# Optimization experiments

Measured on AMD Instinct MI355X. Metric: run time of the kernel, lower is better.

Reference implementation:

```python
import jax, jax.numpy as jnp
import numpy as np

IN_DIM = 256
HID = 512
PAT = 10
B = 512
BN_EPS = 1e-5


def setup_inputs() -> dict:
    key = jax.random.key(0)
    ks = jax.random.split(key, 16)
    s = 0.05
    return {
        "x": jax.random.normal(ks[0], (B, IN_DIM), jnp.float32),
        # pattern_detector params
        "W1": jax.random.normal(ks[1], (HID, IN_DIM), jnp.float32) * s,
        "b1": jax.random.normal(ks[2], (HID,), jnp.float32) * s,
        "bn_gamma": 1.0 + jax.random.normal(ks[3], (HID,), jnp.float32) * s,
        "bn_beta": jax.random.normal(ks[4], (HID,), jnp.float32) * s,
        "bn_mean": jax.random.normal(ks[5], (HID,), jnp.float32) * s,
        "bn_var": jnp.ones((HID,), jnp.float32),
        "W2": jax.random.normal(ks[6], (HID // 2, HID), jnp.float32) * s,
        "b2": jax.random.normal(ks[7], (HID // 2,), jnp.float32) * s,
        "W3": jax.random.normal(ks[8], (PAT, HID // 2), jnp.float32) * s,
        "b3": jax.random.normal(ks[9], (PAT,), jnp.float32) * s,
        # similarity_layer params; first Linear weight [HID, 2*IN_DIM] split into
        # the half acting on x_i (Ws1_a) and the half acting on x_j (Ws1_b)
        "Ws1_a": jax.random.normal(ks[10], (HID, IN_DIM), jnp.float32) * s,
        "Ws1_b": jax.random.normal(ks[11], (HID, IN_DIM), jnp.float32) * s,
        "bs1": jax.random.normal(ks[12], (HID,), jnp.float32) * s,
        "ws2": jax.random.normal(ks[13], (HID,), jnp.float32) * s,
        "bs2": jax.random.normal(ks[14], (), jnp.float32) * s,
    }


def reference(x, W1, b1, bn_gamma, bn_beta, bn_mean, bn_var, W2, b2, W3, b3,
              Ws1_a, Ws1_b, bs1, ws2, bs2):
    # --- pattern_detector MLP (eval mode: BN uses running stats, dropout off) ---
    h = x @ W1.T + b1                                    # [B, HID]
    h = bn_gamma * (h - bn_mean) * jax.lax.rsqrt(bn_var + BN_EPS) + bn_beta
    h = jax.nn.relu(h)
    h2 = jax.nn.relu(h @ W2.T + b2)                      # [B, HID//2]
    pattern_scores = h2 @ W3.T + b3                      # [B, PAT]
    pattern_probs = jax.nn.softmax(pattern_scores, axis=-1)

    # --- pairwise similarity: sim(i,j) = MLP(concat(x_i, x_j)) ---
    # Linear([x_i; x_j]) = x_i @ Ws1_a^T + x_j @ Ws1_b^T + bs1, so precompute
    # the two GEMMs and broadcast-add instead of materializing [B,B,2*IN_DIM].
    A = x @ Ws1_a.T                                      # [B, HID]
    C = x @ Ws1_b.T                                      # [B, HID]
    hid = jax.nn.relu(A[:, None, :] + C[None, :, :] + bs1)  # [B, B, HID]
    logits = hid @ ws2 + bs2                             # [B, B]
    sim_full = jax.nn.sigmoid(logits)
    # Original loops i<j only and mirrors, diagonal stays 0. Results are
    # detached (.item()) in torch, so stop_gradient for faithfulness.
    iu = jnp.triu(jnp.ones((x.shape[0], x.shape[0]), sim_full.dtype), k=1)
    S = sim_full * iu
    similarities = jax.lax.stop_gradient(S + S.T)

    return pattern_probs, pattern_scores, similarities
```

## Files before the change

kernel.cpp:

```cpp
#include <hip/hip_runtime.h>
#include <math.h>

#define BN_EPS 1e-5f

typedef _Float16 half2v __attribute__((ext_vector_type(2)));
typedef _Float16 half8v __attribute__((ext_vector_type(8)));
typedef __fp16 fp16x8 __attribute__((ext_vector_type(8)));
typedef float floatx4 __attribute__((ext_vector_type(4)));

__device__ __forceinline__ float fdot2(half2v a, half2v b, float c) {
    return __builtin_amdgcn_fdot2(a, b, c, false);
}
__device__ __forceinline__ half2v cvt2(float a, float b) {
    return __builtin_bit_cast(half2v, __builtin_amdgcn_cvt_pkrtz(a, b));
}
__device__ __forceinline__ floatx4 mfma16(half8v a, half8v b, floatx4 c) {
    return __builtin_amdgcn_mfma_f32_16x16x32_f16(
        __builtin_bit_cast(fp16x8, a), __builtin_bit_cast(fp16x8, b), c, 0, 0, 0);
}

__global__ __launch_bounds__(256) void fused3_mfma(
    const float* __restrict__ x,
    const float* __restrict__ W1, const float* __restrict__ b1,
    const float* __restrict__ g, const float* __restrict__ be,
    const float* __restrict__ mu, const float* __restrict__ va,
    const float* __restrict__ Wa, const float* __restrict__ bs1,
    const float* __restrict__ Wb,
    _Float16* __restrict__ h16, _Float16* __restrict__ A16,
    _Float16* __restrict__ C16)
{
    __shared__ _Float16 Xs[64][264];
    __shared__ _Float16 Ws[32][264];

    const int t  = threadIdx.x;
    const int n0 = blockIdx.x * 32;
    const int m0 = blockIdx.y * 64;
    const int z  = blockIdx.z;
    const float* __restrict__ Wp = (z == 0) ? W1 : (z == 1 ? Wa : Wb);

    #pragma unroll
    for (int i = 0; i < 16; ++i) {
        const int cidx = t + i * 256;
        const int row = cidx >> 6;
        const int c4  = cidx & 63;
        const float4 v = *(const float4*)&x[(m0 + row) * 256 + c4 * 4];
        *(half2v*)&Xs[row][c4 * 4 + 0] = cvt2(v.x, v.y);
        *(half2v*)&Xs[row][c4 * 4 + 2] = cvt2(v.z, v.w);
    }
    #pragma unroll
    for (int i = 0; i < 8; ++i) {
        const int cidx = t + i * 256;
        const int row = cidx >> 6;
        const int c4  = cidx & 63;
        const float4 v = *(const float4*)&Wp[(n0 + row) * 256 + c4 * 4];
        *(half2v*)&Ws[row][c4 * 4 + 0] = cvt2(v.x, v.y);
        *(half2v*)&Ws[row][c4 * 4 + 2] = cvt2(v.z, v.w);
    }
    __syncthreads();

    const int wave = t >> 6;
    const int lane = t & 63;
    const int wy = wave >> 1, wx = wave & 1;
    const int lrow = lane & 15;
    const int quad = lane >> 4;
    const int kq = quad * 8;

    floatx4 acc[2] = {{0.f, 0.f, 0.f, 0.f}, {0.f, 0.f, 0.f, 0.f}};

    #pragma unroll
    for (int kc = 0; kc < 256; kc += 32) {
        const half8v a0 = *(const half8v*)&Xs[wy * 32 + lrow][kc + kq];
        const half8v a1 = *(const half8v*)&Xs[wy * 32 + 16 + lrow][kc + kq];
        const half8v b0 = *(const half8v*)&Ws[wx * 16 + lrow][kc + kq];
        acc[0] = mfma16(a0, b0, acc[0]);
        acc[1] = mfma16(a1, b0, acc[1]);
    }

    const int n = n0 + wx * 16 + lrow;
    float scale, off;
    if (z == 0) {
        const float s = g[n] * rsqrtf(va[n] + BN_EPS);
        scale = s;
        off = (b1[n] - mu[n]) * s + be[n];
    } else if (z == 1) {
        scale = 1.f;
        off = bs1[n];
    } else {
        scale = 1.f;
        off = 0.f;
    }
    _Float16* __restrict__ dst = (z == 0) ? h16 : (z == 1 ? A16 : C16);
    #pragma unroll
    for (int mi = 0; mi < 2; ++mi) {
        #pragma unroll
        for (int r = 0; r < 4; ++r) {
            const int m = m0 + wy * 32 + mi * 16 + quad * 4 + r;
            float v = acc[mi][r] * scale + off;
            if (z == 0) v = fmaxf(v, 0.f);
            dst[m * 512 + n] = (_Float16)v;
        }
    }
}

__global__ __launch_bounds__(256) void h2_mfma(
    const _Float16* __restrict__ h16, const float* __restrict__ W2,
    const float* __restrict__ b2, float* __restrict__ h2o)
{
    __shared__ _Float16 Xs[32][520];
    __shared__ _Float16 Ws[32][520];

    const int t  = threadIdx.x;
    const int n0 = blockIdx.x * 32;
    const int m0 = blockIdx.y * 32;

    #pragma unroll
    for (int i = 0; i < 8; ++i) {
        const int cidx = t + i * 256;
        const int row = cidx >> 6;
        const int c8  = cidx & 63;
        const float4 v = *(const float4*)&h16[(m0 + row) * 512 + c8 * 8];
        *(half8v*)&Xs[row][c8 * 8] = __builtin_bit_cast(half8v, v);
    }
    #pragma unroll
    for (int i = 0; i < 8; ++i) {
        const int cidx = t + i * 256;
        const int row = cidx >> 6;
        const int c8  = cidx & 63;
        const float4 v0 = *(const float4*)&W2[(n0 + row) * 512 + c8 * 8];
        const float4 v1 = *(const float4*)&W2[(n0 + row) * 512 + c8 * 8 + 4];
        *(half2v*)&Ws[row][c8 * 8 + 0] = cvt2(v0.x, v0.y);
        *(half2v*)&Ws[row][c8 * 8 + 2] = cvt2(v0.z, v0.w);
        *(half2v*)&Ws[row][c8 * 8 + 4] = cvt2(v1.x, v1.y);
        *(half2v*)&Ws[row][c8 * 8 + 6] = cvt2(v1.z, v1.w);
    }
    __syncthreads();

    const int wave = t >> 6;
    const int lane = t & 63;
    const int wy = wave >> 1, wx = wave & 1;
    const int lrow = lane & 15;
    const int quad = lane >> 4;
    const int kq = quad * 8;

    floatx4 acc = {0.f, 0.f, 0.f, 0.f};
    #pragma unroll
    for (int kc = 0; kc < 512; kc += 32) {
        const half8v a = *(const half8v*)&Xs[wy * 16 + lrow][kc + kq];
        const half8v b = *(const half8v*)&Ws[wx * 16 + lrow][kc + kq];
        acc = mfma16(a, b, acc);
    }

    const int n = n0 + wx * 16 + lrow;
    const float bb = b2[n];
    #pragma unroll
    for (int r = 0; r < 4; ++r) {
        const int m = m0 + wy * 16 + quad * 4 + r;
        h2o[m * 256 + n] = fmaxf(acc[r] + bb, 0.f);
    }
}

__global__ __launch_bounds__(256) void tail_kernel(
    const float* __restrict__ h2, const float* __restrict__ W3,
    const float* __restrict__ b3,
    const _Float16* __restrict__ A16, const _Float16* __restrict__ C16,
    const float* __restrict__ ws2, const float* __restrict__ bs2,
    float* __restrict__ out)
{
    __shared__ _Float16 Rs[16][520];
    __shared__ _Float16 Qs[16][520];
    __shared__ half2v wsh[256];
    __shared__ float Tt[16][17];

    const int bid = blockIdx.x;
    const int t   = threadIdx.x;

    if (bid >= 528) {
        const int lane = t & 63;
        const int r = (bid - 528) * 4 + (t >> 6);

        float p[10];
        #pragma unroll
        for (int q = 0; q < 10; ++q) p[q] = 0.f;
        #pragma unroll
        for (int kk = 0; kk < 4; ++kk) {
            const int k = lane + kk * 64;
            const float hv = h2[r * 256 + k];
            #pragma unroll
            for (int q = 0; q < 10; ++q)
                p[q] = fmaf(hv, W3[q * 256 + k], p[q]);
        }
        #pragma unroll
        for (int q = 0; q < 10; ++q) {
            #pragma unroll
            for (int off = 32; off > 0; off >>= 1)
                p[q] += __shfl_down(p[q], off);
        }
        if (lane == 0) {
            float s[10], m = -1e30f;
            #pragma unroll
            for (int q = 0; q < 10; ++q) { s[q] = p[q] + b3[q]; m = fmaxf(m, s[q]); }
            float e[10], sum = 0.f;
            #pragma unroll
            for (int q = 0; q < 10; ++q) { e[q] = __expf(s[q] - m); sum += e[q]; }
            const float inv = 1.f / sum;
            #pragma unroll
            for (int q = 0; q < 10; ++q) {
                out[r * 10 + q] = e[q] * inv;
                out[5120 + r * 10 + q] = s[q];
            }
        }
        return;
    }

    float* __restrict__ S = out + 10240;
    int jt = 0;
    {
        int b = bid;
        while ((jt + 1) * (jt + 2) / 2 <= b) ++jt;
    }
    const int it = bid - jt * (jt + 1) / 2;
    const int r0 = it * 16, q0 = jt * 16;
    const bool diag = (it == jt);

    {
        half2v w;
        w.x = (_Float16)ws2[2 * t];
        w.y = (_Float16)ws2[2 * t + 1];
        wsh[t] = w;
    }
    #pragma unroll
    for (int i = 0; i < 4; ++i) {
        const int cidx = t + i * 256;
        const int row = cidx >> 6;
        const int c8  = cidx & 63;
        const float4 vr = *(const float4*)&A16[(r0 + row) * 512 + c8 * 8];
        const float4 vq = *(const float4*)&C16[(q0 + row) * 512 + c8 * 8];
        *(half8v*)&Rs[row][c8 * 8] = __builtin_bit_cast(half8v, vr);
        *(half8v*)&Qs[row][c8 * 8] = __builtin_bit_cast(half8v, vq);
    }
    __syncthreads();

    const int tx = t & 15, ty = t >> 4;
    const half2v* rp = (const half2v*)&Rs[ty][0];
    const half2v* qp = (const half2v*)&Qs[tx][0];
    const half2v z2 = {(_Float16)0, (_Float16)0};

    float a0 = 0.f;
    #pragma unroll 8
    for (int k2 = 0; k2 < 256; ++k2) {
        a0 = fdot2(__builtin_elementwise_max(rp[k2] + qp[k2], z2), wsh[k2], a0);
    }
    const float v = 1.f / (1.f + __expf(-(a0 + bs2[0])));

    Tt[ty][tx] = v;
    __syncthreads();

    if (diag) {
        const int r = r0 + ty, q = q0 + tx;
        const float o = (r < q) ? Tt[ty][tx] : (r > q ? Tt[tx][ty] : 0.f);
        S[r * 512 + q] = o;
    } else {
        S[(r0 + ty) * 512 + q0 + tx] = v;
        S[(q0 + ty) * 512 + r0 + tx] = Tt[tx][ty];
    }
}

extern "C" void kernel_launch(void* const* d_in, const int* in_sizes, int n_in,
                              void* d_out, int out_size, void* d_ws, size_t ws_size,
                              hipStream_t stream)
{
    const float* x   = (const float*)d_in[0];
    const float* W1  = (const float*)d_in[1];
    const float* b1  = (const float*)d_in[2];
    const float* g   = (const float*)d_in[3];
    const float* be  = (const float*)d_in[4];
    const float* mu  = (const float*)d_in[5];
    const float* va  = (const float*)d_in[6];
    const float* W2  = (const float*)d_in[7];
    const float* b2  = (const float*)d_in[8];
    const float* W3  = (const float*)d_in[9];
    const float* b3  = (const float*)d_in[10];
    const float* Wa  = (const float*)d_in[11];
    const float* Wb  = (const float*)d_in[12];
    const float* bs1 = (const float*)d_in[13];
    const float* ws2 = (const float*)d_in[14];
    const float* bs2 = (const float*)d_in[15];

    float* out = (float*)d_out;
    _Float16* h16 = (_Float16*)d_ws;
    float* h2 = (float*)(h16 + 512 * 512);
    _Float16* A16 = (_Float16*)(h2 + 512 * 256);
    _Float16* C16 = A16 + 512 * 512;

    fused3_mfma<<<dim3(16, 8, 3), 256, 0, stream>>>(x, W1, b1, g, be, mu, va,
                                                    Wa, bs1, Wb, h16, A16, C16);
    h2_mfma<<<dim3(8, 16), 256, 0, stream>>>(h16, W2, b2, h2);
    tail_kernel<<<656, 256, 0, stream>>>(h2, W3, b3, A16, C16, ws2, bs2, out);
}
```

Measured before the change: 98.98 us.

## Fuse h2 GEMM and pattern head into similarity tail kernel

Removes the separate h2_mfma launch and the h2 global buffer. The first 32 blocks of the tail kernel now compute h2 for 16 rows each, by looping over all 256 output columns in 16-column chunks with split-K MFMA across waves, and then apply W3 and softmax in place. This saves a kernel launch and a global round trip. In exchange, those 32 blocks each reload and convert all of W2 serially with two syncs per chunk, which could make them the critical path.

```diff
diff --git a/kernel.cpp b/kernel.cpp
--- a/kernel.cpp
+++ b/kernel.cpp
@@ -102,106 +102,103 @@
     }
 }
 
-__global__ __launch_bounds__(256) void h2_mfma(
-    const _Float16* __restrict__ h16, const float* __restrict__ W2,
-    const float* __restrict__ b2, float* __restrict__ h2o)
-{
-    __shared__ _Float16 Xs[32][520];
-    __shared__ _Float16 Ws[32][520];
-
-    const int t  = threadIdx.x;
-    const int n0 = blockIdx.x * 32;
-    const int m0 = blockIdx.y * 32;
-
-    #pragma unroll
-    for (int i = 0; i < 8; ++i) {
-        const int cidx = t + i * 256;
-        const int row = cidx >> 6;
-        const int c8  = cidx & 63;
-        const float4 v = *(const float4*)&h16[(m0 + row) * 512 + c8 * 8];
-        *(half8v*)&Xs[row][c8 * 8] = __builtin_bit_cast(half8v, v);
-    }
-    #pragma unroll
-    for (int i = 0; i < 8; ++i) {
-        const int cidx = t + i * 256;
-        const int row = cidx >> 6;
-        const int c8  = cidx & 63;
-        const float4 v0 = *(const float4*)&W2[(n0 + row) * 512 + c8 * 8];
-        const float4 v1 = *(const float4*)&W2[(n0 + row) * 512 + c8 * 8 + 4];
-        *(half2v*)&Ws[row][c8 * 8 + 0] = cvt2(v0.x, v0.y);
-        *(half2v*)&Ws[row][c8 * 8 + 2] = cvt2(v0.z, v0.w);
-        *(half2v*)&Ws[row][c8 * 8 + 4] = cvt2(v1.x, v1.y);
-        *(half2v*)&Ws[row][c8 * 8 + 6] = cvt2(v1.z, v1.w);
-    }
-    __syncthreads();
-
-    const int wave = t >> 6;
-    const int lane = t & 63;
-    const int wy = wave >> 1, wx = wave & 1;
-    const int lrow = lane & 15;
-    const int quad = lane >> 4;
-    const int kq = quad * 8;
-
-    floatx4 acc = {0.f, 0.f, 0.f, 0.f};
-    #pragma unroll
-    for (int kc = 0; kc < 512; kc += 32) {
-        const half8v a = *(const half8v*)&Xs[wy * 16 + lrow][kc + kq];
-        const half8v b = *(const half8v*)&Ws[wx * 16 + lrow][kc + kq];
-        acc = mfma16(a, b, acc);
-    }
-
-    const int n = n0 + wx * 16 + lrow;
-    const float bb = b2[n];
-    #pragma unroll
-    for (int r = 0; r < 4; ++r) {
-        const int m = m0 + wy * 16 + quad * 4 + r;
-        h2o[m * 256 + n] = fmaxf(acc[r] + bb, 0.f);
-    }
-}
-
-__global__ __launch_bounds__(256) void tail_kernel(
-    const float* __restrict__ h2, const float* __restrict__ W3,
-    const float* __restrict__ b3,
+__global__ __launch_bounds__(256) void tail2_kernel(
+    const _Float16* __restrict__ h16,
+    const float* __restrict__ W2, const float* __restrict__ b2,
+    const float* __restrict__ W3, const float* __restrict__ b3,
     const _Float16* __restrict__ A16, const _Float16* __restrict__ C16,
     const float* __restrict__ ws2, const float* __restrict__ bs2,
     float* __restrict__ out)
 {
-    __shared__ _Float16 Rs[16][520];
-    __shared__ _Float16 Qs[16][520];
+    __shared__ _Float16 RsQs[2][16][520];
     __shared__ half2v wsh[256];
     __shared__ float Tt[16][17];
+    __shared__ float Hp[4][16][17];
 
     const int bid = blockIdx.x;
     const int t   = threadIdx.x;
 
-    if (bid >= 528) {
+    if (bid < 32) {
+        const int m0   = bid * 16;
+        const int wave = t >> 6;
         const int lane = t & 63;
-        const int r = (bid - 528) * 4 + (t >> 6);
+        const int lrow = lane & 15;
+        const int quad = lane >> 4;
+        const int m  = t >> 4;
+        const int nn = t & 15;
+
+        #pragma unroll
+        for (int i = 0; i < 4; ++i) {
+            const int cidx = t + i * 256;
+            const int row = cidx >> 6;
+            const int c8  = cidx & 63;
+            *(half8v*)&RsQs[0][row][c8 * 8] =
+                *(const half8v*)&h16[(m0 + row) * 512 + c8 * 8];
+        }
+
+        float hr[16];
+        #pragma unroll
+        for (int c = 0; c < 16; ++c) {
+            #pragma unroll
+            for (int i = 0; i < 4; ++i) {
+                const int cidx = t + i * 256;
+                const int row = cidx >> 6;
+                const int c8  = cidx & 63;
+                const float4 v0 = *(const float4*)&W2[(c * 16 + row) * 512 + c8 * 8];
+                const float4 v1 = *(const float4*)&W2[(c * 16 + row) * 512 + c8 * 8 + 4];
+                *(half2v*)&RsQs[1][row][c8 * 8 + 0] = cvt2(v0.x, v0.y);
+                *(half2v*)&RsQs[1][row][c8 * 8 + 2] = cvt2(v0.z, v0.w);
+                *(half2v*)&RsQs[1][row][c8 * 8 + 4] = cvt2(v1.x, v1.y);
+                *(half2v*)&RsQs[1][row][c8 * 8 + 6] = cvt2(v1.z, v1.w);
+            }
+            __syncthreads();
+
+            floatx4 acc = {0.f, 0.f, 0.f, 0.f};
+            #pragma unroll
+            for (int j = 0; j < 4; ++j) {
+                const int kk = wave * 128 + j * 32 + quad * 8;
+                const half8v a = *(const half8v*)&RsQs[0][lrow][kk];
+                const half8v b = *(const half8v*)&RsQs[1][lrow][kk];
+                acc = mfma16(a, b, acc);
+            }
+            #pragma unroll
+            for (int r = 0; r < 4; ++r)
+                Hp[wave][quad * 4 + r][lrow] = acc[r];
+            __syncthreads();
+
+            const float s = Hp[0][m][nn] + Hp[1][m][nn] +
+                            Hp[2][m][nn] + Hp[3][m][nn] + b2[c * 16 + nn];
+            hr[c] = fmaxf(s, 0.f);
+        }
+
+        float* W3f = (float*)&RsQs[0][0][0];
+        #pragma unroll
+        for (int i = 0; i < 10; ++i) W3f[t + i * 256] = W3[t + i * 256];
+        __syncthreads();
 
         float p[10];
         #pragma unroll
-        for (int q = 0; q < 10; ++q) p[q] = 0.f;
-        #pragma unroll
-        for (int kk = 0; kk < 4; ++kk) {
-            const int k = lane + kk * 64;
-            const float hv = h2[r * 256 + k];
-            #pragma unroll
-            for (int q = 0; q < 10; ++q)
-                p[q] = fmaf(hv, W3[q * 256 + k], p[q]);
-        }
-        #pragma unroll
         for (int q = 0; q < 10; ++q) {
-            #pragma unroll
-            for (int off = 32; off > 0; off >>= 1)
-                p[q] += __shfl_down(p[q], off);
-        }
-        if (lane == 0) {
-            float s[10], m = -1e30f;
-            #pragma unroll
-            for (int q = 0; q < 10; ++q) { s[q] = p[q] + b3[q]; m = fmaxf(m, s[q]); }
+            float a = 0.f;
+            #pragma unroll
+            for (int c = 0; c < 16; ++c)
+                a = fmaf(hr[c], W3f[q * 256 + c * 16 + nn], a);
+            p[q] = a;
+        }
+        #pragma unroll
+        for (int q = 0; q < 10; ++q) {
+            #pragma unroll
+            for (int off = 8; off > 0; off >>= 1)
+                p[q] += __shfl_xor(p[q], off);
+        }
+        if (nn == 0) {
+            const int r = m0 + m;
+            float s[10], mx = -1e30f;
+            #pragma unroll
+            for (int q = 0; q < 10; ++q) { s[q] = p[q] + b3[q]; mx = fmaxf(mx, s[q]); }
             float e[10], sum = 0.f;
             #pragma unroll
-            for (int q = 0; q < 10; ++q) { e[q] = __expf(s[q] - m); sum += e[q]; }
+            for (int q = 0; q < 10; ++q) { e[q] = __expf(s[q] - mx); sum += e[q]; }
             const float inv = 1.f / sum;
             #pragma unroll
             for (int q = 0; q < 10; ++q) {
@@ -213,12 +210,12 @@
     }
 
     float* __restrict__ S = out + 10240;
+    const int b = bid - 32;
     int jt = 0;
     {
-        int b = bid;
         while ((jt + 1) * (jt + 2) / 2 <= b) ++jt;
     }
-    const int it = bid - jt * (jt + 1) / 2;
+    const int it = b - jt * (jt + 1) / 2;
     const int r0 = it * 16, q0 = jt * 16;
     const bool diag = (it == jt);
 
@@ -235,14 +232,14 @@
         const int c8  = cidx & 63;
         const float4 vr = *(const float4*)&A16[(r0 + row) * 512 + c8 * 8];
         const float4 vq = *(const float4*)&C16[(q0 + row) * 512 + c8 * 8];
-        *(half8v*)&Rs[row][c8 * 8] = __builtin_bit_cast(half8v, vr);
-        *(half8v*)&Qs[row][c8 * 8] = __builtin_bit_cast(half8v, vq);
+        *(half8v*)&RsQs[0][row][c8 * 8] = __builtin_bit_cast(half8v, vr);
+        *(half8v*)&RsQs[1][row][c8 * 8] = __builtin_bit_cast(half8v, vq);
     }
     __syncthreads();
 
     const int tx = t & 15, ty = t >> 4;
-    const half2v* rp = (const half2v*)&Rs[ty][0];
-    const half2v* qp = (const half2v*)&Qs[tx][0];
+    const half2v* rp = (const half2v*)&RsQs[0][ty][0];
+    const half2v* qp = (const half2v*)&RsQs[1][tx][0];
     const half2v z2 = {(_Float16)0, (_Float16)0};
 
     float a0 = 0.f;
@@ -288,12 +285,11 @@
 
     float* out = (float*)d_out;
     _Float16* h16 = (_Float16*)d_ws;
-    float* h2 = (float*)(h16 + 512 * 512);
-    _Float16* A16 = (_Float16*)(h2 + 512 * 256);
+    _Float16* A16 = h16 + 512 * 512;
     _Float16* C16 = A16 + 512 * 512;
 
     fused3_mfma<<<dim3(16, 8, 3), 256, 0, stream>>>(x, W1, b1, g, be, mu, va,
                                                     Wa, bs1, Wb, h16, A16, C16);
-    h2_mfma<<<dim3(8, 16), 256, 0, stream>>>(h16, W2, b2, h2);
-    tail_kernel<<<656, 256, 0, stream>>>(h2, W3, b3, A16, C16, ws2, bs2, out);
-}
+    tail2_kernel<<<560, 256, 0, stream>>>(h16, W2, b2, W3, b3, A16, C16,
+                                          ws2, bs2, out);
+}
```

New measurement: 120.0 us. 1.21x slower.

## Enlarge pairwise similarity tiles to 32x32 with 4 outputs per thread

Applied to the files above, without the earlier changes.

The pairwise similarity tail kernel now handles 32x32 tiles instead of 16x16, which cuts the upper-triangular block count from 528 to 136. Each thread computes four outputs that share one row of A and the ws2 weights. Operands are loaded as half4 vectors, so each LDS read feeds more packed dot products. The aim is to reduce LDS traffic and per-block overhead in the dominant B*B*HID loop, at the cost of fewer blocks (264 total), which may underfill the GPU, plus more registers and shared memory per block.

```diff
diff --git a/kernel.cpp b/kernel.cpp
--- a/kernel.cpp
+++ b/kernel.cpp
@@ -4,6 +4,7 @@
 #define BN_EPS 1e-5f
 
 typedef _Float16 half2v __attribute__((ext_vector_type(2)));
+typedef _Float16 half4v __attribute__((ext_vector_type(4)));
 typedef _Float16 half8v __attribute__((ext_vector_type(8)));
 typedef __fp16 fp16x8 __attribute__((ext_vector_type(8)));
 typedef float floatx4 __attribute__((ext_vector_type(4)));
@@ -159,24 +160,24 @@
     }
 }
 
-__global__ __launch_bounds__(256) void tail_kernel(
+__global__ __launch_bounds__(256) void tail3_kernel(
     const float* __restrict__ h2, const float* __restrict__ W3,
     const float* __restrict__ b3,
     const _Float16* __restrict__ A16, const _Float16* __restrict__ C16,
     const float* __restrict__ ws2, const float* __restrict__ bs2,
     float* __restrict__ out)
 {
-    __shared__ _Float16 Rs[16][520];
-    __shared__ _Float16 Qs[16][520];
-    __shared__ half2v wsh[256];
-    __shared__ float Tt[16][17];
+    __shared__ __align__(16) _Float16 Rs[32][520];
+    __shared__ __align__(16) _Float16 Qs[32][520];
+    __shared__ __align__(16) _Float16 wshh[512];
+    __shared__ float T[32][33];
 
     const int bid = blockIdx.x;
     const int t   = threadIdx.x;
 
-    if (bid >= 528) {
+    if (bid >= 136) {
         const int lane = t & 63;
-        const int r = (bid - 528) * 4 + (t >> 6);
+        const int r = (bid - 136) * 4 + (t >> 6);
 
         float p[10];
         #pragma unroll
@@ -219,49 +220,101 @@
         while ((jt + 1) * (jt + 2) / 2 <= b) ++jt;
     }
     const int it = bid - jt * (jt + 1) / 2;
-    const int r0 = it * 16, q0 = jt * 16;
+    const int r0 = it * 32, q0 = jt * 32;
     const bool diag = (it == jt);
 
     {
-        half2v w;
-        w.x = (_Float16)ws2[2 * t];
-        w.y = (_Float16)ws2[2 * t + 1];
-        wsh[t] = w;
-    }
-    #pragma unroll
-    for (int i = 0; i < 4; ++i) {
+        const float2 wv = *(const float2*)&ws2[2 * t];
+        *(half2v*)&wshh[2 * t] = cvt2(wv.x, wv.y);
+    }
+    #pragma unroll
+    for (int i = 0; i < 8; ++i) {
         const int cidx = t + i * 256;
         const int row = cidx >> 6;
         const int c8  = cidx & 63;
-        const float4 vr = *(const float4*)&A16[(r0 + row) * 512 + c8 * 8];
-        const float4 vq = *(const float4*)&C16[(q0 + row) * 512 + c8 * 8];
-        *(half8v*)&Rs[row][c8 * 8] = __builtin_bit_cast(half8v, vr);
-        *(half8v*)&Qs[row][c8 * 8] = __builtin_bit_cast(half8v, vq);
+        *(half8v*)&Rs[row][c8 * 8] =
+            *(const half8v*)&A16[(r0 + row) * 512 + c8 * 8];
+        *(half8v*)&Qs[row][c8 * 8] =
+            *(const half8v*)&C16[(q0 + row) * 512 + c8 * 8];
     }
     __syncthreads();
 
-    const int tx = t & 15, ty = t >> 4;
-    const half2v* rp = (const half2v*)&Rs[ty][0];
-    const half2v* qp = (const half2v*)&Qs[tx][0];
+    const int wave = t >> 6;
+    const int lane = t & 63;
+    const int ly = lane >> 3;
+    const int lx = lane & 7;
+    const int row = wave * 8 + ly;
+
+    const half4v* ap  = (const half4v*)&Rs[row][0];
+    const half4v* wp  = (const half4v*)&wshh[0];
+    const half4v* q0p = (const half4v*)&Qs[lx +  0][0];
+    const half4v* q1p = (const half4v*)&Qs[lx +  8][0];
+    const half4v* q2p = (const half4v*)&Qs[lx + 16][0];
+    const half4v* q3p = (const half4v*)&Qs[lx + 24][0];
+
     const half2v z2 = {(_Float16)0, (_Float16)0};
-
-    float a0 = 0.f;
-    #pragma unroll 8
-    for (int k2 = 0; k2 < 256; ++k2) {
-        a0 = fdot2(__builtin_elementwise_max(rp[k2] + qp[k2], z2), wsh[k2], a0);
-    }
-    const float v = 1.f / (1.f + __expf(-(a0 + bs2[0])));
-
-    Tt[ty][tx] = v;
+    float acc0 = 0.f, acc1 = 0.f, acc2 = 0.f, acc3 = 0.f;
+
+    #pragma unroll 16
+    for (int k4 = 0; k4 < 128; ++k4) {
+        const half4v a4 = ap[k4];
+        const half4v w4 = wp[k4];
+        const half2v alo = __builtin_shufflevector(a4, a4, 0, 1);
+        const half2v ahi = __builtin_shufflevector(a4, a4, 2, 3);
+        const half2v wlo = __builtin_shufflevector(w4, w4, 0, 1);
+        const half2v whi = __builtin_shufflevector(w4, w4, 2, 3);
+        half4v q;
+        q = q0p[k4];
+        acc0 = fdot2(__builtin_elementwise_max(
+                   alo + __builtin_shufflevector(q, q, 0, 1), z2), wlo, acc0);
+        acc0 = fdot2(__builtin_elementwise_max(
+                   ahi + __builtin_shufflevector(q, q, 2, 3), z2), whi, acc0);
+        q = q1p[k4];
+        acc1 = fdot2(__builtin_elementwise_max(
+                   alo + __builtin_shufflevector(q, q, 0, 1), z2), wlo, acc1);
+        acc1 = fdot2(__builtin_elementwise_max(
+                   ahi + __builtin_shufflevector(q, q, 2, 3), z2), whi, acc1);
+        q = q2p[k4];
+        acc2 = fdot2(__builtin_elementwise_max(
+                   alo + __builtin_shufflevector(q, q, 0, 1), z2), wlo, acc2);
+        acc2 = fdot2(__builtin_elementwise_max(
+                   ahi + __builtin_shufflevector(q, q, 2, 3), z2), whi, acc2);
+        q = q3p[k4];
+        acc3 = fdot2(__builtin_elementwise_max(
+                   alo + __builtin_shufflevector(q, q, 0, 1), z2), wlo, acc3);
+        acc3 = fdot2(__builtin_elementwise_max(
+                   ahi + __builtin_shufflevector(q, q, 2, 3), z2), whi, acc3);
+    }
+
+    const float bb = bs2[0];
+    T[row][lx +  0] = 1.f / (1.f + __expf(-(acc0 + bb)));
+    T[row][lx +  8] = 1.f / (1.f + __expf(-(acc1 + bb)));
+    T[row][lx + 16] = 1.f / (1.f + __expf(-(acc2 + bb)));
+    T[row][lx + 24] = 1.f / (1.f + __expf(-(acc3 + bb)));
     __syncthreads();
 
+    const int ty = t >> 4, tx = t & 15;
     if (diag) {
-        const int r = r0 + ty, q = q0 + tx;
-        const float o = (r < q) ? Tt[ty][tx] : (r > q ? Tt[tx][ty] : 0.f);
-        S[r * 512 + q] = o;
+        #pragma unroll
+        for (int dy = 0; dy < 2; ++dy) {
+            #pragma unroll
+            for (int dx = 0; dx < 2; ++dx) {
+                const int i = ty + dy * 16, jj = tx + dx * 16;
+                const float o = (i < jj) ? T[i][jj]
+                                         : (i > jj ? T[jj][i] : 0.f);
+                S[(r0 + i) * 512 + q0 + jj] = o;
+            }
+        }
     } else {
-        S[(r0 + ty) * 512 + q0 + tx] = v;
-        S[(q0 + ty) * 512 + r0 + tx] = Tt[tx][ty];
+        #pragma unroll
+        for (int dy = 0; dy < 2; ++dy) {
+            #pragma unroll
+            for (int dx = 0; dx < 2; ++dx) {
+                const int i = ty + dy * 16, jj = tx + dx * 16;
+                S[(r0 + i) * 512 + q0 + jj] = T[i][jj];
+                S[(q0 + i) * 512 + r0 + jj] = T[jj][i];
+            }
+        }
     }
 }
 
@@ -295,5 +348,5 @@
     fused3_mfma<<<dim3(16, 8, 3), 256, 0, stream>>>(x, W1, b1, g, be, mu, va,
                                                     Wa, bs1, Wb, h16, A16, C16);
     h2_mfma<<<dim3(8, 16), 256, 0, stream>>>(h16, W2, b2, h2);
-    tail_kernel<<<656, 256, 0, stream>>>(h2, W3, b3, A16, C16, ws2, bs2, out);
-}
+    tail3_kernel<<<264, 256, 0, stream>>>(h2, W3, b3, A16, C16, ws2, bs2, out);
+}
```

After: 103.3 us. +4.3%, slower.
